# Kernel tuning notes

Hardware: AMD Instinct MI355X
Metric: run time of the kernel (lower is better)

The kernel has to match this reference:

```python
import jax, jax.numpy as jnp
import numpy as np

B, C, IC, H, W = 4, 64, 32, 128, 128


def _conv1x1(x, w, b):
    # x: [b,c,h,w], w: [o,c], b: [o]
    return jnp.einsum('bchw,oc->bohw', x, w) + b[None, :, None, None]


def _maxpool2(x):
    b, c, h, w = x.shape
    return x.reshape(b, c, h // 2, 2, w // 2, 2).max(axis=(3, 5))


def setup_inputs() -> dict:
    key = jax.random.key(0)
    ks = jax.random.split(key, 11)
    sc = 0.05
    return {
        'target': jax.random.normal(ks[0], (B, C, H, W), jnp.float32),
        'ref': jax.random.normal(ks[1], (B, C, H, W), jnp.float32),
        'ref_align': jax.random.normal(ks[2], (B, C, H, W), jnp.float32),
        'theta_w': jax.random.normal(ks[3], (IC, C), jnp.float32) * sc,
        'theta_b': jax.random.normal(ks[4], (IC,), jnp.float32) * sc,
        'phi_w': jax.random.normal(ks[5], (IC, C), jnp.float32) * sc,
        'phi_b': jax.random.normal(ks[6], (IC,), jnp.float32) * sc,
        'g_w': jax.random.normal(ks[7], (IC, C), jnp.float32) * sc,
        'g_b': jax.random.normal(ks[8], (IC,), jnp.float32) * sc,
        'W_w': jax.random.normal(ks[9], (C, IC), jnp.float32) * sc,
        'W_b': jax.random.normal(ks[10], (C,), jnp.float32) * sc,
    }


def reference(target, ref, ref_align, theta_w, theta_b, phi_w, phi_b, g_w, g_b, W_w, W_b):
    b, c, h, w = target.shape
    N = h * w
    # phi, g: 1x1 conv then 2x2 maxpool -> [b, ic, N/4]
    phi = _maxpool2(_conv1x1(ref, phi_w, phi_b)).reshape(b, -1, N // 4)
    g = _maxpool2(_conv1x1(ref_align, g_w, g_b)).reshape(b, -1, N // 4)
    theta = _conv1x1(target, theta_w, theta_b).reshape(b, -1, N)  # [b, ic, N]
    # softmax-free attention: s [b, N, N/4]
    s = jnp.einsum('bin,bim->bnm', theta, phi) / N
    y = jnp.einsum('bnm,bim->bin', s, g)  # [b, ic, N]
    y = y.reshape(b, -1, h, w)
    return _conv1x1(y, W_w, W_b) + target
```

## Files before the change

### kernel.cpp

```cpp
#include <hip/hip_runtime.h>

#define Bn  4
#define Cc  64
#define ICc 32
#define Hh  128
#define Ww  128
#define Nn  (Hh*Ww)
#define Hp  (Hh/2)
#define Wp  (Ww/2)
#define Mm  (Hp*Wp)
#define Sg  8

__global__ __launch_bounds__(128) void conv_pool_kernel(
    const float* __restrict__ ref, const float* __restrict__ ref_align,
    const float* __restrict__ phi_w, const float* __restrict__ phi_b,
    const float* __restrict__ g_w,   const float* __restrict__ g_b,
    float* __restrict__ P, float* __restrict__ G)
{
    const int z   = blockIdx.z;
    const int inp = z & 1;
    const int icb = (z >> 1) * (ICc / 2);
    const float* in   = inp ? ref_align : ref;
    const float* wmat = (inp ? g_w : phi_w) + icb * Cc;
    const float* bias = (inp ? g_b : phi_b) + icb;
    float* outp       = inp ? G : P;

    __shared__ float sw[(ICc / 2) * Cc];
    __shared__ float sb[ICc / 2];
    for (int idx = threadIdx.x; idx < (ICc / 2) * Cc; idx += 128) sw[idx] = wmat[idx];
    if (threadIdx.x < ICc / 2) sb[threadIdx.x] = bias[threadIdx.x];
    __syncthreads();

    const int tid = threadIdx.x;
    const int pw  = tid >> 1;
    const int r   = tid & 1;
    const int ph  = blockIdx.x;
    const int b   = blockIdx.y;
    const int hh  = 2 * ph + r;

    const float2* xrow = (const float2*)(in + ((size_t)b * Cc * Hh + hh) * Ww);
    const int cstride2 = (Hh * Ww) / 2;

    float acc0[ICc / 2], acc1[ICc / 2];
    #pragma unroll
    for (int i = 0; i < ICc / 2; ++i) { acc0[i] = sb[i]; acc1[i] = sb[i]; }

    #pragma unroll 4
    for (int c = 0; c < Cc; ++c) {
        float2 v = xrow[c * cstride2 + pw];
        #pragma unroll
        for (int i = 0; i < ICc / 2; ++i) {
            acc0[i] = fmaf(sw[i * Cc + c], v.x, acc0[i]);
            acc1[i] = fmaf(sw[i * Cc + c], v.y, acc1[i]);
        }
    }

    const int m = ph * Wp + pw;
    #pragma unroll
    for (int i = 0; i < ICc / 2; ++i) {
        float mx = fmaxf(acc0[i], acc1[i]);
        mx = fmaxf(mx, __shfl_xor(mx, 1, 64));
        if (r == 0) outp[((size_t)(b * ICc + icb + i)) * Mm + m] = mx;
    }
}

__global__ __launch_bounds__(256) void gram_kernel(
    const float* __restrict__ P, const float* __restrict__ G,
    float* __restrict__ Apart)
{
    const int i = blockIdx.x, b = blockIdx.y, s = blockIdx.z;
    const float* Gi = G + ((size_t)(b * ICc + i)) * Mm;
    const float* Pb = P + (size_t)b * ICc * Mm;
    const int mbase = s * (Mm / Sg);

    float acc[ICc];
    #pragma unroll
    for (int j = 0; j < ICc; ++j) acc[j] = 0.f;

    #pragma unroll
    for (int k = 0; k < (Mm / Sg) / 256; ++k) {
        int m = mbase + k * 256 + threadIdx.x;
        float gv = Gi[m];
        #pragma unroll
        for (int j = 0; j < ICc; ++j) acc[j] = fmaf(gv, Pb[j * Mm + m], acc[j]);
    }

    #pragma unroll
    for (int j = 0; j < ICc; ++j) {
        #pragma unroll
        for (int off = 32; off > 0; off >>= 1)
            acc[j] += __shfl_xor(acc[j], off, 64);
    }

    __shared__ float red[4][ICc];
    const int lane = threadIdx.x & 63, wid = threadIdx.x >> 6;
    if (lane == 0)
        for (int j = 0; j < ICc; ++j) red[wid][j] = acc[j];
    __syncthreads();

    if (threadIdx.x < ICc) {
        float sum = red[0][threadIdx.x] + red[1][threadIdx.x]
                  + red[2][threadIdx.x] + red[3][threadIdx.x];
        Apart[(((size_t)b * Sg + s) * ICc + i) * ICc + threadIdx.x] = sum;
    }
}

__global__ __launch_bounds__(64) void combine_kernel(
    const float* __restrict__ Apart, const float* __restrict__ theta_w,
    const float* __restrict__ theta_b, const float* __restrict__ W_w,
    const float* __restrict__ W_b, float* __restrict__ Mp)
{
    const int b = blockIdx.x, o = threadIdx.x;
    __shared__ float sA[ICc * ICc];
    for (int idx = threadIdx.x; idx < ICc * ICc; idx += 64) {
        float sum = 0.f;
        #pragma unroll
        for (int s = 0; s < Sg; ++s)
            sum += Apart[((size_t)b * Sg + s) * ICc * ICc + idx];
        sA[idx] = sum;
    }
    __syncthreads();

    float T[ICc];
    #pragma unroll
    for (int j = 0; j < ICc; ++j) T[j] = 0.f;
    for (int i = 0; i < ICc; ++i) {
        float wv = W_w[o * ICc + i];
        #pragma unroll
        for (int j = 0; j < ICc; ++j) T[j] = fmaf(wv, sA[i * ICc + j], T[j]);
    }

    const float invN = 1.f / (float)Nn;
    float* Mb = Mp + (size_t)b * (Cc * Cc + Cc);
    for (int c = 0; c < Cc; ++c) {
        float s = 0.f;
        #pragma unroll
        for (int j = 0; j < ICc; ++j) s = fmaf(T[j], theta_w[j * Cc + c], s);
        Mb[o * Cc + c] = s * invN + (o == c ? 1.f : 0.f);
    }
    float v = 0.f;
    #pragma unroll
    for (int j = 0; j < ICc; ++j) v = fmaf(T[j], theta_b[j], v);
    Mb[Cc * Cc + o] = v * invN + W_b[o];
}

__global__ __launch_bounds__(256) void apply_kernel(
    const float* __restrict__ x, const float* __restrict__ Mp, float* __restrict__ out)
{
    const int b = blockIdx.y;
    const int obase = blockIdx.z * 8;
    const float* Mb = Mp + (size_t)b * (Cc * Cc + Cc);

    __shared__ float sM[8 * Cc];
    __shared__ float sv[8];
    for (int idx = threadIdx.x; idx < 8 * Cc; idx += 256)
        sM[idx] = Mb[(obase + (idx >> 6)) * Cc + (idx & 63)];
    if (threadIdx.x < 8) sv[threadIdx.x] = Mb[Cc * Cc + obase + threadIdx.x];
    __syncthreads();

    const int n2 = blockIdx.x * 256 + threadIdx.x;
    const float2* xb = (const float2*)(x + (size_t)b * Cc * Nn);
    float2*       ob = (float2*)(out + (size_t)b * Cc * Nn);

    float accx[8], accy[8];
    #pragma unroll
    for (int i = 0; i < 8; ++i) { accx[i] = sv[i]; accy[i] = sv[i]; }

    #pragma unroll 4
    for (int c = 0; c < Cc; ++c) {
        float2 xv = xb[c * (Nn / 2) + n2];
        #pragma unroll
        for (int i = 0; i < 8; ++i) {
            float w = sM[i * Cc + c];
            accx[i] = fmaf(w, xv.x, accx[i]);
            accy[i] = fmaf(w, xv.y, accy[i]);
        }
    }

    #pragma unroll
    for (int i = 0; i < 8; ++i) {
        float2 o2; o2.x = accx[i]; o2.y = accy[i];
        ob[(obase + i) * (Nn / 2) + n2] = o2;
    }
}

extern "C" void kernel_launch(void* const* d_in, const int* in_sizes, int n_in,
                              void* d_out, int out_size, void* d_ws, size_t ws_size,
                              hipStream_t stream) {
    const float* target    = (const float*)d_in[0];
    const float* ref       = (const float*)d_in[1];
    const float* ref_align = (const float*)d_in[2];
    const float* theta_w   = (const float*)d_in[3];
    const float* theta_b   = (const float*)d_in[4];
    const float* phi_w     = (const float*)d_in[5];
    const float* phi_b     = (const float*)d_in[6];
    const float* g_w       = (const float*)d_in[7];
    const float* g_b       = (const float*)d_in[8];
    const float* W_w       = (const float*)d_in[9];
    const float* W_b       = (const float*)d_in[10];
    float* out = (float*)d_out;

    float* ws    = (float*)d_ws;
    float* P     = ws;
    float* G     = P + (size_t)Bn * ICc * Mm;
    float* Apart = G + (size_t)Bn * ICc * Mm;
    float* Mp    = Apart + (size_t)Bn * Sg * ICc * ICc;

    conv_pool_kernel<<<dim3(Hp, Bn, 4), 128, 0, stream>>>(ref, ref_align,
                                                          phi_w, phi_b, g_w, g_b, P, G);
    gram_kernel<<<dim3(ICc, Bn, Sg), 256, 0, stream>>>(P, G, Apart);
    combine_kernel<<<Bn, 64, 0, stream>>>(Apart, theta_w, theta_b, W_w, W_b, Mp);
    apply_kernel<<<dim3(Nn / 512, Bn, 8), 256, 0, stream>>>(target, Mp, out);
}
```

Baseline: 154.0 us.

## Fuse combine into apply kernel and halve output channels per block

The tiny single-wave-per-batch combine kernel is removed. Each apply block now redundantly reduces the partial Gram matrices and computes its own 4 rows of the folded 64x64 matrix in shared memory. Both conv_pool and apply are split into twice as many blocks, with fewer output channels each, to raise parallelism and cut register pressure. The cost is redundant Apart reads and small matmuls in every apply block, and more repeated reads of the input activations across blocks.

New measurement: 151.0 us. Within noise of the previous version (-1.9%).

```diff
diff --git a/kernel.cpp b/kernel.cpp
--- a/kernel.cpp
+++ b/kernel.cpp
@@ -19,16 +19,16 @@
 {
     const int z   = blockIdx.z;
     const int inp = z & 1;
-    const int icb = (z >> 1) * (ICc / 2);
+    const int icb = (z >> 1) * 8;
     const float* in   = inp ? ref_align : ref;
     const float* wmat = (inp ? g_w : phi_w) + icb * Cc;
     const float* bias = (inp ? g_b : phi_b) + icb;
     float* outp       = inp ? G : P;
 
-    __shared__ float sw[(ICc / 2) * Cc];
-    __shared__ float sb[ICc / 2];
-    for (int idx = threadIdx.x; idx < (ICc / 2) * Cc; idx += 128) sw[idx] = wmat[idx];
-    if (threadIdx.x < ICc / 2) sb[threadIdx.x] = bias[threadIdx.x];
+    __shared__ float sw[8 * Cc];
+    __shared__ float sb[8];
+    for (int idx = threadIdx.x; idx < 8 * Cc; idx += 128) sw[idx] = wmat[idx];
+    if (threadIdx.x < 8) sb[threadIdx.x] = bias[threadIdx.x];
     __syncthreads();
 
     const int tid = threadIdx.x;
@@ -41,15 +41,15 @@
     const float2* xrow = (const float2*)(in + ((size_t)b * Cc * Hh + hh) * Ww);
     const int cstride2 = (Hh * Ww) / 2;
 
-    float acc0[ICc / 2], acc1[ICc / 2];
-    #pragma unroll
-    for (int i = 0; i < ICc / 2; ++i) { acc0[i] = sb[i]; acc1[i] = sb[i]; }
-
-    #pragma unroll 4
+    float acc0[8], acc1[8];
+    #pragma unroll
+    for (int i = 0; i < 8; ++i) { acc0[i] = sb[i]; acc1[i] = sb[i]; }
+
+    #pragma unroll 8
     for (int c = 0; c < Cc; ++c) {
         float2 v = xrow[c * cstride2 + pw];
         #pragma unroll
-        for (int i = 0; i < ICc / 2; ++i) {
+        for (int i = 0; i < 8; ++i) {
             acc0[i] = fmaf(sw[i * Cc + c], v.x, acc0[i]);
             acc1[i] = fmaf(sw[i * Cc + c], v.y, acc1[i]);
         }
@@ -57,7 +57,7 @@
 
     const int m = ph * Wp + pw;
     #pragma unroll
-    for (int i = 0; i < ICc / 2; ++i) {
+    for (int i = 0; i < 8; ++i) {
         float mx = fmaxf(acc0[i], acc1[i]);
         mx = fmaxf(mx, __shfl_xor(mx, 1, 64));
         if (r == 0) outp[((size_t)(b * ICc + icb + i)) * Mm + m] = mx;
@@ -105,72 +105,68 @@
     }
 }
 
-__global__ __launch_bounds__(64) void combine_kernel(
-    const float* __restrict__ Apart, const float* __restrict__ theta_w,
-    const float* __restrict__ theta_b, const float* __restrict__ W_w,
-    const float* __restrict__ W_b, float* __restrict__ Mp)
+__global__ __launch_bounds__(256) void apply_kernel(
+    const float* __restrict__ x, const float* __restrict__ Apart,
+    const float* __restrict__ theta_w, const float* __restrict__ theta_b,
+    const float* __restrict__ W_w,     const float* __restrict__ W_b,
+    float* __restrict__ out)
 {
-    const int b = blockIdx.x, o = threadIdx.x;
+    const int b     = blockIdx.y;
+    const int obase = blockIdx.z * 4;
+
     __shared__ float sA[ICc * ICc];
-    for (int idx = threadIdx.x; idx < ICc * ICc; idx += 64) {
+    __shared__ float sT[4 * ICc];
+    __shared__ float sM[4 * Cc];
+    __shared__ float sv[4];
+
+    const float* Ab = Apart + (size_t)b * Sg * ICc * ICc;
+    for (int idx = threadIdx.x; idx < ICc * ICc; idx += 256) {
         float sum = 0.f;
         #pragma unroll
-        for (int s = 0; s < Sg; ++s)
-            sum += Apart[((size_t)b * Sg + s) * ICc * ICc + idx];
+        for (int s = 0; s < Sg; ++s) sum += Ab[s * ICc * ICc + idx];
         sA[idx] = sum;
     }
     __syncthreads();
 
-    float T[ICc];
-    #pragma unroll
-    for (int j = 0; j < ICc; ++j) T[j] = 0.f;
-    for (int i = 0; i < ICc; ++i) {
-        float wv = W_w[o * ICc + i];
-        #pragma unroll
-        for (int j = 0; j < ICc; ++j) T[j] = fmaf(wv, sA[i * ICc + j], T[j]);
-    }
+    if (threadIdx.x < 4 * ICc) {
+        const int ol = threadIdx.x >> 5, j = threadIdx.x & 31;
+        const float* wr = W_w + (obase + ol) * ICc;
+        float t = 0.f;
+        #pragma unroll
+        for (int i = 0; i < ICc; ++i) t = fmaf(wr[i], sA[i * ICc + j], t);
+        sT[ol * ICc + j] = t;
+    }
+    __syncthreads();
 
     const float invN = 1.f / (float)Nn;
-    float* Mb = Mp + (size_t)b * (Cc * Cc + Cc);
-    for (int c = 0; c < Cc; ++c) {
+    {
+        const int ol = threadIdx.x >> 6, c = threadIdx.x & 63;
         float s = 0.f;
         #pragma unroll
-        for (int j = 0; j < ICc; ++j) s = fmaf(T[j], theta_w[j * Cc + c], s);
-        Mb[o * Cc + c] = s * invN + (o == c ? 1.f : 0.f);
-    }
-    float v = 0.f;
-    #pragma unroll
-    for (int j = 0; j < ICc; ++j) v = fmaf(T[j], theta_b[j], v);
-    Mb[Cc * Cc + o] = v * invN + W_b[o];
-}
-
-__global__ __launch_bounds__(256) void apply_kernel(
-    const float* __restrict__ x, const float* __restrict__ Mp, float* __restrict__ out)
-{
-    const int b = blockIdx.y;
-    const int obase = blockIdx.z * 8;
-    const float* Mb = Mp + (size_t)b * (Cc * Cc + Cc);
-
-    __shared__ float sM[8 * Cc];
-    __shared__ float sv[8];
-    for (int idx = threadIdx.x; idx < 8 * Cc; idx += 256)
-        sM[idx] = Mb[(obase + (idx >> 6)) * Cc + (idx & 63)];
-    if (threadIdx.x < 8) sv[threadIdx.x] = Mb[Cc * Cc + obase + threadIdx.x];
+        for (int j = 0; j < ICc; ++j) s = fmaf(sT[ol * ICc + j], theta_w[j * Cc + c], s);
+        sM[ol * Cc + c] = s * invN + ((obase + ol) == c ? 1.f : 0.f);
+        if (threadIdx.x < 4) {
+            float v = 0.f;
+            #pragma unroll
+            for (int j = 0; j < ICc; ++j) v = fmaf(sT[threadIdx.x * ICc + j], theta_b[j], v);
+            sv[threadIdx.x] = v * invN + W_b[obase + threadIdx.x];
+        }
+    }
     __syncthreads();
 
     const int n2 = blockIdx.x * 256 + threadIdx.x;
     const float2* xb = (const float2*)(x + (size_t)b * Cc * Nn);
     float2*       ob = (float2*)(out + (size_t)b * Cc * Nn);
 
-    float accx[8], accy[8];
-    #pragma unroll
-    for (int i = 0; i < 8; ++i) { accx[i] = sv[i]; accy[i] = sv[i]; }
-
-    #pragma unroll 4
+    float accx[4], accy[4];
+    #pragma unroll
+    for (int i = 0; i < 4; ++i) { accx[i] = sv[i]; accy[i] = sv[i]; }
+
+    #pragma unroll 8
     for (int c = 0; c < Cc; ++c) {
         float2 xv = xb[c * (Nn / 2) + n2];
         #pragma unroll
-        for (int i = 0; i < 8; ++i) {
+        for (int i = 0; i < 4; ++i) {
             float w = sM[i * Cc + c];
             accx[i] = fmaf(w, xv.x, accx[i]);
             accy[i] = fmaf(w, xv.y, accy[i]);
@@ -178,7 +174,7 @@
     }
 
     #pragma unroll
-    for (int i = 0; i < 8; ++i) {
+    for (int i = 0; i < 4; ++i) {
         float2 o2; o2.x = accx[i]; o2.y = accy[i];
         ob[(obase + i) * (Nn / 2) + n2] = o2;
     }
@@ -204,11 +200,11 @@
     float* P     = ws;
     float* G     = P + (size_t)Bn * ICc * Mm;
     float* Apart = G + (size_t)Bn * ICc * Mm;
-    float* Mp    = Apart + (size_t)Bn * Sg * ICc * ICc;
-
-    conv_pool_kernel<<<dim3(Hp, Bn, 4), 128, 0, stream>>>(ref, ref_align,
+
+    conv_pool_kernel<<<dim3(Hp, Bn, 8), 128, 0, stream>>>(ref, ref_align,
                                                           phi_w, phi_b, g_w, g_b, P, G);
     gram_kernel<<<dim3(ICc, Bn, Sg), 256, 0, stream>>>(P, G, Apart);
-    combine_kernel<<<Bn, 64, 0, stream>>>(Apart, theta_w, theta_b, W_w, W_b, Mp);
-    apply_kernel<<<dim3(Nn / 512, Bn, 8), 256, 0, stream>>>(target, Mp, out);
-}
+    apply_kernel<<<dim3(Nn / 512, Bn, 16), 256, 0, stream>>>(target, Apart,
+                                                             theta_w, theta_b,
+                                                             W_w, W_b, out);
+}
```
